# Kernel tuning notes

Measured on AMD Instinct MI355X. Metric: run time of the kernel, lower is better.

The kernel has to match this reference:

```python
import jax, jax.numpy as jnp
import numpy as np

SHAPE = (192, 192, 192)


def _trilinear_sample(img, z, y, x):
    # img: [B,C,D,H,W]; z,y,x: [B,D,H,W] absolute voxel coords (align_corners=True,
    # zero padding outside the volume, matching F.grid_sample defaults in vroc).
    B, C, D, H, W = img.shape
    imgf = img.reshape(B, C, -1)
    z0 = jnp.floor(z); y0 = jnp.floor(y); x0 = jnp.floor(x)
    wz = z - z0; wy = y - y0; wx = x - x0
    z0i = z0.astype(jnp.int32); y0i = y0.astype(jnp.int32); x0i = x0.astype(jnp.int32)
    z1i = z0i + 1; y1i = y0i + 1; x1i = x0i + 1

    def gather(iz, iy, ix):
        valid = ((iz >= 0) & (iz < D) & (iy >= 0) & (iy < H) & (ix >= 0) & (ix < W))
        lin = ((jnp.clip(iz, 0, D - 1) * H + jnp.clip(iy, 0, H - 1)) * W
               + jnp.clip(ix, 0, W - 1)).reshape(B, 1, -1)
        v = jnp.take_along_axis(imgf, jnp.broadcast_to(lin, (B, C, D * H * W)), axis=2)
        return v.reshape(B, C, D, H, W) * valid.reshape(B, 1, D, H, W).astype(img.dtype)

    def w(a, b, c):
        return (a * b * c)[:, None]  # [B,1,D,H,W]

    out = (gather(z0i, y0i, x0i) * w(1 - wz, 1 - wy, 1 - wx)
           + gather(z0i, y0i, x1i) * w(1 - wz, 1 - wy, wx)
           + gather(z0i, y1i, x0i) * w(1 - wz, wy, 1 - wx)
           + gather(z0i, y1i, x1i) * w(1 - wz, wy, wx)
           + gather(z1i, y0i, x0i) * w(wz, 1 - wy, 1 - wx)
           + gather(z1i, y0i, x1i) * w(wz, 1 - wy, wx)
           + gather(z1i, y1i, x0i) * w(wz, wy, 1 - wx)
           + gather(z1i, y1i, x1i) * w(wz, wy, wx))
    return out


def _warp(moving_image, vector_field):
    # SpatialTransformer: identity grid + displacement (voxel units), trilinear sample.
    B, C, D, H, W = moving_image.shape
    dt = moving_image.dtype
    gz, gy, gx = jnp.meshgrid(jnp.arange(D, dtype=dt), jnp.arange(H, dtype=dt),
                              jnp.arange(W, dtype=dt), indexing='ij')
    z = gz[None] + vector_field[:, 0]
    y = gy[None] + vector_field[:, 1]
    x = gx[None] + vector_field[:, 2]
    return _trilinear_sample(moving_image, z, y, x)


def setup_inputs() -> dict:
    key = jax.random.key(0)
    k1, k2, k3, k4 = jax.random.split(key, 4)
    D, H, W = SHAPE
    moving_image = jax.random.normal(k1, (1, 1, D, H, W), dtype=jnp.float32)
    vector_field = jax.random.normal(k2, (1, 3, D, H, W), dtype=jnp.float32) * 3.0
    fixed_image = jax.random.normal(k3, (1, 1, D, H, W), dtype=jnp.float32)
    fixed_image_mask = jax.random.randint(k4, (1, 1, D, H, W), 0, 2).astype(bool)
    return {"moving_image": moving_image, "vector_field": vector_field,
            "fixed_image": fixed_image, "fixed_image_mask": fixed_image_mask}


def reference(moving_image, vector_field, fixed_image, fixed_image_mask):
    warped = _warp(moving_image, vector_field)
    m = fixed_image_mask.astype(warped.dtype)
    sq = (warped - fixed_image) ** 2
    # F.mse_loss(warped[mask], fixed[mask]) == mean of squared diff over masked voxels
    return jnp.sum(sq * m) / jnp.maximum(jnp.sum(m), 1.0)
```

## Files before the change

### kernel.cpp

```cpp
#include <hip/hip_runtime.h>
#include <hip/hip_fp16.h>

#define DD 192
#define HH 192
#define WW 192
#define NVOX (DD * HH * WW)

#define RSX 32
#define RSY 33
#define RSZ 33
#define ROWD 16
#define SLABD (RSY * ROWD)
#define RTOTH (RSX * RSY * RSZ)
#define RTOTD (RTOTH / 2)
#define NCHUNK (RTOTH / 8)
#define CHSLAB (RSY * 4)
#define NT 1024
#define NROUND ((NCHUNK + NT - 1) / NT)
#define NTILE 1728
#define GRID 256

#define AS1 __attribute__((address_space(1)))
#define AS3 __attribute__((address_space(3)))

#define WAITCNT(n) asm volatile("s_waitcnt vmcnt(" #n ")" ::: "memory")

typedef float f32x4 __attribute__((ext_vector_type(4)));
typedef int   i32x4 __attribute__((ext_vector_type(4)));

__global__ __launch_bounds__(256) void conv_fp16(
    const float4* __restrict__ in, int4* __restrict__ out)
{
    const int i = blockIdx.x * 256 + threadIdx.x;
    const float4 a = in[2 * i];
    const float4 b = in[2 * i + 1];
    __half2 h0 = __floats2half2_rn(a.x, a.y);
    __half2 h1 = __floats2half2_rn(a.z, a.w);
    __half2 h2 = __floats2half2_rn(b.x, b.y);
    __half2 h3 = __floats2half2_rn(b.z, b.w);
    int4 o;
    o.x = *(int*)&h0; o.y = *(int*)&h1; o.z = *(int*)&h2; o.w = *(int*)&h3;
    out[i] = o;
}

struct Streams { f32x4 dz, dy, dx, f; i32x4 m; };

__device__ __forceinline__ void tile_coords_oct(
    int n, int OX, int OY, int OZ, int& tx, int& ty, int& tz)
{
    const int ox = n / 36;
    const int r  = n - ox * 36;
    const int oy = r / 6;
    tx = OX + ox;
    ty = OY + oy;
    tz = OZ + (r - oy * 6);
}

__device__ __forceinline__ void stage_tile(
    const ushort* __restrict__ movh, const ushort* __restrict__ zbuf,
    uint* sbufd, int x_lo, int y_lo, int z_lo, int tid)
{
    ushort* sbuf = (ushort*)sbufd;
    #pragma unroll
    for (int i = 0; i < NROUND; ++i) {
        const int q = tid + i * NT;
        if (q < NCHUNK) {
            const int rz = q / CHSLAB;
            const int rem = q - rz * CHSLAB;
            const int ry = rem >> 2;
            const int k  = rem & 3;
            const int gz = z_lo + rz, gy = y_lo + ry, gx = x_lo + 8 * k;
            const bool valid = ((unsigned)gz < DD) & ((unsigned)gy < HH) &
                               ((unsigned)gx < WW);
            const ushort* src = valid ? (movh + ((gz * HH + gy) * WW + gx)) : zbuf;
            const int qb = i * NT + (tid & ~63);
            __builtin_amdgcn_global_load_lds((AS1 void*)src,
                                             (AS3 void*)(sbuf + 8 * qb), 16, 0, 0);
        }
    }
}

__device__ __forceinline__ Streams prefetch_streams(
    const float* __restrict__ vf, const float* __restrict__ fix,
    const int* __restrict__ mask, int base)
{
    Streams s;
    s.dz = __builtin_nontemporal_load((const f32x4*)(vf + base));
    s.dy = __builtin_nontemporal_load((const f32x4*)(vf + NVOX + base));
    s.dx = __builtin_nontemporal_load((const f32x4*)(vf + 2 * NVOX + base));
    s.f  = __builtin_nontemporal_load((const f32x4*)(fix + base));
    s.m  = __builtin_nontemporal_load((const i32x4*)(mask + base));
    return s;
}

__device__ __forceinline__ void sample_accum(
    const uint* sdw, const float* __restrict__ mov,
    int gz, int gy, int gx, float dz, float dy, float dx,
    float f, int m, int x_lo, int y_lo, int z_lo,
    float& sq, float& cnt)
{
    const float z = (float)gz + dz, y = (float)gy + dy, x = (float)gx + dx;
    const float z0f = floorf(z), y0f = floorf(y), x0f = floorf(x);
    const float wz = z - z0f, wy = y - y0f, wx = x - x0f;
    const int z0 = (int)z0f, y0 = (int)y0f, x0 = (int)x0f;
    const int z0l = z0 - z_lo, y0l = y0 - y_lo, x0l = x0 - x_lo;
    const bool inbox = ((unsigned)z0l < RSZ - 1) & ((unsigned)y0l < RSY - 1) &
                       ((unsigned)x0l < RSX - 1);

    float v000, v001, v010, v011, v100, v101, v110, v111;
    if (inbox) {
        const int o = z0l * SLABD + y0l * ROWD + (x0l >> 1);
        const bool odd = (x0l & 1) != 0;
        const uint a00 = sdw[o];
        const uint b00 = sdw[o + 1];
        const uint a01 = sdw[o + ROWD];
        const uint b01 = sdw[o + ROWD + 1];
        const uint a10 = sdw[o + SLABD];
        const uint b10 = sdw[o + SLABD + 1];
        const uint a11 = sdw[o + SLABD + ROWD];
        const uint b11 = sdw[o + SLABD + ROWD + 1];
        auto pr = [&](uint A, uint B, float& l, float& r) {
            const float2 fa = __half22float2(*(const __half2*)&A);
            const float fb = __low2float(*(const __half2*)&B);
            l = odd ? fa.y : fa.x;
            r = odd ? fb   : fa.y;
        };
        pr(a00, b00, v000, v001);
        pr(a01, b01, v010, v011);
        pr(a10, b10, v100, v101);
        pr(a11, b11, v110, v111);
    } else {
        const int z1 = z0 + 1, y1 = y0 + 1, x1 = x0 + 1;
        const bool zi0 = (unsigned)z0 < DD, zi1 = (unsigned)z1 < DD;
        const bool yi0 = (unsigned)y0 < HH, yi1 = (unsigned)y1 < HH;
        const bool xi0 = (unsigned)x0 < WW, xi1 = (unsigned)x1 < WW;
        auto ld = [&](int iz, int iy, int ix, bool ok) -> float {
            return ok ? mov[(iz * HH + iy) * WW + ix] : 0.0f;
        };
        v000 = ld(z0, y0, x0, zi0 & yi0 & xi0);
        v001 = ld(z0, y0, x1, zi0 & yi0 & xi1);
        v010 = ld(z0, y1, x0, zi0 & yi1 & xi0);
        v011 = ld(z0, y1, x1, zi0 & yi1 & xi1);
        v100 = ld(z1, y0, x0, zi1 & yi0 & xi0);
        v101 = ld(z1, y0, x1, zi1 & yi0 & xi1);
        v110 = ld(z1, y1, x0, zi1 & yi1 & xi0);
        v111 = ld(z1, y1, x1, zi1 & yi1 & xi1);
    }

    const float c00 = v000 + (v001 - v000) * wx;
    const float c01 = v010 + (v011 - v010) * wx;
    const float c10 = v100 + (v101 - v100) * wx;
    const float c11 = v110 + (v111 - v110) * wx;
    const float c0 = c00 + (c01 - c00) * wy;
    const float c1 = c10 + (c11 - c10) * wy;
    const float warped = c0 + (c1 - c0) * wz;

    const float mm = (m != 0) ? 1.0f : 0.0f;
    const float diff = warped - f;
    sq += diff * diff * mm;
    cnt += mm;
}

__global__ __launch_bounds__(NT) void warp_mse_persist(
    const ushort* __restrict__ movh,
    const float* __restrict__ mov,
    const float* __restrict__ vf,
    const float* __restrict__ fix,
    const int* __restrict__ mask,
    const ushort* __restrict__ zbuf,
    float* __restrict__ acc,
    float* __restrict__ out)
{
    __shared__ uint sbufd[2][RTOTD];
    __shared__ float s_sq[16], s_cnt[16];

    const int tid = threadIdx.x;
    const int b = blockIdx.x;
    const int xcd = b & 7;
    const int w   = b >> 3;
    const int start = w * 6 + min(w, 24);
    const int cnt_t = 6 + (w < 24 ? 1 : 0);
    const int OX = (xcd & 1) * 6;
    const int OY = ((xcd >> 1) & 1) * 6;
    const int OZ = ((xcd >> 2) & 1) * 6;

    const int lxg = (tid & 3) * 4;
    const int ly  = (tid >> 2) & 15;
    const int lz  = tid >> 6;

    float sq = 0.0f, cntm = 0.0f;

    int tx, ty, tz;
    tile_coords_oct(start, OX, OY, OZ, tx, ty, tz);
    stage_tile(movh, zbuf, sbufd[0], tx * 16 - 8, ty * 16 - 8, tz * 16 - 8, tid);
    Streams Scur = prefetch_streams(vf, fix, mask,
        ((tz * 16 + lz) * HH + ty * 16 + ly) * WW + tx * 16 + lxg);
    Streams Snxt = Scur;
    if (cnt_t > 1) {
        int nx, ny, nz;
        tile_coords_oct(start + 1, OX, OY, OZ, nx, ny, nz);
        stage_tile(movh, zbuf, sbufd[1], nx * 16 - 8, ny * 16 - 8, nz * 16 - 8, tid);
        Snxt = prefetch_streams(vf, fix, mask,
            ((nz * 16 + lz) * HH + ny * 16 + ly) * WW + nx * 16 + lxg);
        WAITCNT(14);
    } else {
        WAITCNT(5);
    }
    __builtin_amdgcn_s_barrier();
    __builtin_amdgcn_sched_barrier(0);

    for (int k = 0; k < cnt_t; ++k) {
        const int cur = k & 1;
        int cx, cy, cz;
        tile_coords_oct(start + k, OX, OY, OZ, cx, cy, cz);
        const int x_lo = cx * 16 - 8, y_lo = cy * 16 - 8, z_lo = cz * 16 - 8;
        const int gz = cz * 16 + lz, gy = cy * 16 + ly, gx0 = cx * 16 + lxg;
        const uint* sdw = sbufd[cur];

        sample_accum(sdw, mov, gz, gy, gx0,     Scur.dz.x, Scur.dy.x, Scur.dx.x,
                     Scur.f.x, Scur.m.x, x_lo, y_lo, z_lo, sq, cntm);
        sample_accum(sdw, mov, gz, gy, gx0 + 1, Scur.dz.y, Scur.dy.y, Scur.dx.y,
                     Scur.f.y, Scur.m.y, x_lo, y_lo, z_lo, sq, cntm);
        sample_accum(sdw, mov, gz, gy, gx0 + 2, Scur.dz.z, Scur.dy.z, Scur.dx.z,
                     Scur.f.z, Scur.m.z, x_lo, y_lo, z_lo, sq, cntm);
        sample_accum(sdw, mov, gz, gy, gx0 + 3, Scur.dz.w, Scur.dy.w, Scur.dx.w,
                     Scur.f.w, Scur.m.w, x_lo, y_lo, z_lo, sq, cntm);

        if (k + 1 < cnt_t) {
            __builtin_amdgcn_sched_barrier(0);
            __builtin_amdgcn_s_barrier();
            Streams Snew = Snxt;
            if (k + 2 < cnt_t) {
                int nx, ny, nz;
                tile_coords_oct(start + k + 2, OX, OY, OZ, nx, ny, nz);
                stage_tile(movh, zbuf, sbufd[cur],
                           nx * 16 - 8, ny * 16 - 8, nz * 16 - 8, tid);
                Snew = prefetch_streams(vf, fix, mask,
                    ((nz * 16 + lz) * HH + ny * 16 + ly) * WW + nx * 16 + lxg);
                WAITCNT(14);
            } else {
                WAITCNT(5);
            }
            __builtin_amdgcn_s_barrier();
            __builtin_amdgcn_sched_barrier(0);
            Scur = Snxt;
            Snxt = Snew;
        }
    }

    #pragma unroll
    for (int off = 32; off > 0; off >>= 1) {
        sq   += __shfl_down(sq, off, 64);
        cntm += __shfl_down(cntm, off, 64);
    }
    const int lane = tid & 63;
    const int wid = tid >> 6;
    if (lane == 0) { s_sq[wid] = sq; s_cnt[wid] = cntm; }
    __syncthreads();
    if (tid == 0) {
        float bsq = 0.0f, bcnt = 0.0f;
        #pragma unroll
        for (int i = 0; i < 16; ++i) { bsq += s_sq[i]; bcnt += s_cnt[i]; }
        atomicAdd(&acc[0], bsq);
        atomicAdd(&acc[1], bcnt);
        __threadfence();
        const unsigned old = atomicAdd((unsigned*)&acc[2], 1u);
        if (old == GRID - 1) {
            __threadfence();
            const float s = atomicAdd(&acc[0], 0.0f);
            const float c = atomicAdd(&acc[1], 0.0f);
            out[0] = s / fmaxf(c, 1.0f);
        }
    }
}

__global__ __launch_bounds__(256) void warp_mse_simple(
    const float* __restrict__ mov, const float* __restrict__ vf,
    const float* __restrict__ fix, const int* __restrict__ mask,
    float* __restrict__ acc)
{
    const int idx = blockIdx.x * 256 + threadIdx.x;
    float sq = 0.0f, cnt = 0.0f;
    if (idx < NVOX) {
        const int w = idx % WW;
        const int t = idx / WW;
        const int h = t % HH;
        const int d = t / HH;
        const float z = (float)d + vf[idx];
        const float y = (float)h + vf[NVOX + idx];
        const float x = (float)w + vf[2 * NVOX + idx];
        const float z0f = floorf(z), y0f = floorf(y), x0f = floorf(x);
        const float wz = z - z0f, wy = y - y0f, wx = x - x0f;
        const int z0 = (int)z0f, y0 = (int)y0f, x0 = (int)x0f;
        const int z1 = z0 + 1, y1 = y0 + 1, x1 = x0 + 1;
        const bool zi0 = (unsigned)z0 < DD, zi1 = (unsigned)z1 < DD;
        const bool yi0 = (unsigned)y0 < HH, yi1 = (unsigned)y1 < HH;
        const bool xi0 = (unsigned)x0 < WW, xi1 = (unsigned)x1 < WW;
        auto ld = [&](int iz, int iy, int ix, bool ok) -> float {
            return ok ? mov[(iz * HH + iy) * WW + ix] : 0.0f;
        };
        const float v000 = ld(z0, y0, x0, zi0 & yi0 & xi0);
        const float v001 = ld(z0, y0, x1, zi0 & yi0 & xi1);
        const float v010 = ld(z0, y1, x0, zi0 & yi1 & xi0);
        const float v011 = ld(z0, y1, x1, zi0 & yi1 & xi1);
        const float v100 = ld(z1, y0, x0, zi1 & yi0 & xi0);
        const float v101 = ld(z1, y0, x1, zi1 & yi0 & xi1);
        const float v110 = ld(z1, y1, x0, zi1 & yi1 & xi0);
        const float v111 = ld(z1, y1, x1, zi1 & yi1 & xi1);
        const float c00 = v000 + (v001 - v000) * wx;
        const float c01 = v010 + (v011 - v010) * wx;
        const float c10 = v100 + (v101 - v100) * wx;
        const float c11 = v110 + (v111 - v110) * wx;
        const float c0 = c00 + (c01 - c00) * wy;
        const float c1 = c10 + (c11 - c10) * wy;
        const float warped = c0 + (c1 - c0) * wz;
        const float m = (mask[idx] != 0) ? 1.0f : 0.0f;
        const float diff = warped - fix[idx];
        sq = diff * diff * m;
        cnt = m;
    }
    #pragma unroll
    for (int off = 32; off > 0; off >>= 1) {
        sq  += __shfl_down(sq, off, 64);
        cnt += __shfl_down(cnt, off, 64);
    }
    __shared__ float s_sq[4], s_cnt[4];
    const int lane = threadIdx.x & 63, wid = threadIdx.x >> 6;
    if (lane == 0) { s_sq[wid] = sq; s_cnt[wid] = cnt; }
    __syncthreads();
    if (threadIdx.x == 0) {
        atomicAdd(&acc[0], s_sq[0] + s_sq[1] + s_sq[2] + s_sq[3]);
        atomicAdd(&acc[1], s_cnt[0] + s_cnt[1] + s_cnt[2] + s_cnt[3]);
    }
}

__global__ void warp_mse_finalize(const float* __restrict__ acc, float* __restrict__ out) {
    out[0] = acc[0] / fmaxf(acc[1], 1.0f);
}

extern "C" void kernel_launch(void* const* d_in, const int* in_sizes, int n_in,
                              void* d_out, int out_size, void* d_ws, size_t ws_size,
                              hipStream_t stream) {
    const float* mov  = (const float*)d_in[0];
    const float* vf   = (const float*)d_in[1];
    const float* fix  = (const float*)d_in[2];
    const int*   mask = (const int*)d_in[3];
    float* acc = (float*)d_ws;
    float* out = (float*)d_out;

    hipMemsetAsync(d_ws, 0, 256, stream);

    const size_t need = 256 + (size_t)NVOX * 2;
    if (ws_size >= need) {
        ushort* movh = (ushort*)((char*)d_ws + 256);
        const ushort* zbuf = (const ushort*)((char*)d_ws + 64);
        conv_fp16<<<NVOX / (256 * 8), 256, 0, stream>>>(
            (const float4*)mov, (int4*)movh);
        warp_mse_persist<<<GRID, NT, 0, stream>>>(movh, mov, vf, fix, mask,
                                                  zbuf, acc, out);
    } else {
        warp_mse_simple<<<(NVOX + 255) / 256, 256, 0, stream>>>(mov, vf, fix, mask, acc);
        warp_mse_finalize<<<1, 1, 0, stream>>>(acc, out);
    }
}
```

Baseline: 233.7 us.

## Reshape tiles to 32x16x8 and use fp16 moving image for fallback gathers

Changes the output tile from 16x16x16 to 32 wide, 16 high and 8 deep. The staged LDS halo region becomes 48x33x25, and the tile indexing, thread mapping and octant offsets are updated to match. The aim is a wider x extent per tile for better coalescing of the streamed inputs and a different halo-to-interior ratio. Out-of-box fallback gathers now read the fp16 copy of the moving image with clamped indices instead of the fp32 copy, which halves the fallback read bytes at some precision cost. The halo volume and per-round chunk counts change, which shifts the LDS footprint and the WAITCNT assumptions that the unchanged vmcnt constants rely on.

New measurement: 217.2 us. -7.1%, faster.

```diff
diff --git a/kernel.cpp b/kernel.cpp
--- a/kernel.cpp
+++ b/kernel.cpp
@@ -6,18 +6,21 @@
 #define WW 192
 #define NVOX (DD * HH * WW)
 
-#define RSX 32
+#define TX 32
+#define TY 16
+#define TZ 8
+#define RSX 48
 #define RSY 33
-#define RSZ 33
-#define ROWD 16
+#define RSZ 25
+#define ROWD 24
 #define SLABD (RSY * ROWD)
 #define RTOTH (RSX * RSY * RSZ)
 #define RTOTD (RTOTH / 2)
 #define NCHUNK (RTOTH / 8)
-#define CHSLAB (RSY * 4)
+#define CHROW 6
+#define CHSLAB (RSY * CHROW)
 #define NT 1024
 #define NROUND ((NCHUNK + NT - 1) / NT)
-#define NTILE 1728
 #define GRID 256
 
 #define AS1 __attribute__((address_space(1)))
@@ -48,12 +51,12 @@
 __device__ __forceinline__ void tile_coords_oct(
     int n, int OX, int OY, int OZ, int& tx, int& ty, int& tz)
 {
-    const int ox = n / 36;
-    const int r  = n - ox * 36;
-    const int oy = r / 6;
+    const int ox = n / 72;
+    const int r  = n - ox * 72;
+    const int oy = r / 12;
     tx = OX + ox;
     ty = OY + oy;
-    tz = OZ + (r - oy * 6);
+    tz = OZ + (r - oy * 12);
 }
 
 __device__ __forceinline__ void stage_tile(
@@ -67,8 +70,8 @@
         if (q < NCHUNK) {
             const int rz = q / CHSLAB;
             const int rem = q - rz * CHSLAB;
-            const int ry = rem >> 2;
-            const int k  = rem & 3;
+            const int ry = rem / CHROW;
+            const int k  = rem - ry * CHROW;
             const int gz = z_lo + rz, gy = y_lo + ry, gx = x_lo + 8 * k;
             const bool valid = ((unsigned)gz < DD) & ((unsigned)gy < HH) &
                                ((unsigned)gx < WW);
@@ -94,7 +97,7 @@
 }
 
 __device__ __forceinline__ void sample_accum(
-    const uint* sdw, const float* __restrict__ mov,
+    const uint* sdw, const ushort* __restrict__ movh,
     int gz, int gy, int gx, float dz, float dy, float dx,
     float f, int m, int x_lo, int y_lo, int z_lo,
     float& sq, float& cnt)
@@ -134,17 +137,21 @@
         const bool zi0 = (unsigned)z0 < DD, zi1 = (unsigned)z1 < DD;
         const bool yi0 = (unsigned)y0 < HH, yi1 = (unsigned)y1 < HH;
         const bool xi0 = (unsigned)x0 < WW, xi1 = (unsigned)x1 < WW;
-        auto ld = [&](int iz, int iy, int ix, bool ok) -> float {
-            return ok ? mov[(iz * HH + iy) * WW + ix] : 0.0f;
-        };
-        v000 = ld(z0, y0, x0, zi0 & yi0 & xi0);
-        v001 = ld(z0, y0, x1, zi0 & yi0 & xi1);
-        v010 = ld(z0, y1, x0, zi0 & yi1 & xi0);
-        v011 = ld(z0, y1, x1, zi0 & yi1 & xi1);
-        v100 = ld(z1, y0, x0, zi1 & yi0 & xi0);
-        v101 = ld(z1, y0, x1, zi1 & yi0 & xi1);
-        v110 = ld(z1, y1, x0, zi1 & yi1 & xi0);
-        v111 = ld(z1, y1, x1, zi1 & yi1 & xi1);
+        const int zc0 = min(max(z0, 0), DD - 1), zc1 = min(max(z1, 0), DD - 1);
+        const int yc0 = min(max(y0, 0), HH - 1), yc1 = min(max(y1, 0), HH - 1);
+        const int xc0 = min(max(x0, 0), WW - 1), xc1 = min(max(x1, 0), WW - 1);
+        const int r00 = (zc0 * HH + yc0) * WW;
+        const int r01 = (zc0 * HH + yc1) * WW;
+        const int r10 = (zc1 * HH + yc0) * WW;
+        const int r11 = (zc1 * HH + yc1) * WW;
+        v000 = (zi0 & yi0 & xi0) ? __half2float(((const __half*)movh)[r00 + xc0]) : 0.0f;
+        v001 = (zi0 & yi0 & xi1) ? __half2float(((const __half*)movh)[r00 + xc1]) : 0.0f;
+        v010 = (zi0 & yi1 & xi0) ? __half2float(((const __half*)movh)[r01 + xc0]) : 0.0f;
+        v011 = (zi0 & yi1 & xi1) ? __half2float(((const __half*)movh)[r01 + xc1]) : 0.0f;
+        v100 = (zi1 & yi0 & xi0) ? __half2float(((const __half*)movh)[r10 + xc0]) : 0.0f;
+        v101 = (zi1 & yi0 & xi1) ? __half2float(((const __half*)movh)[r10 + xc1]) : 0.0f;
+        v110 = (zi1 & yi1 & xi0) ? __half2float(((const __half*)movh)[r11 + xc0]) : 0.0f;
+        v111 = (zi1 & yi1 & xi1) ? __half2float(((const __half*)movh)[r11 + xc1]) : 0.0f;
     }
 
     const float c00 = v000 + (v001 - v000) * wx;
@@ -171,7 +178,7 @@
     float* __restrict__ acc,
     float* __restrict__ out)
 {
-    __shared__ uint sbufd[2][RTOTD];
+    __shared__ uint sbufd[2][RTOTD + 8];
     __shared__ float s_sq[16], s_cnt[16];
 
     const int tid = threadIdx.x;
@@ -180,28 +187,28 @@
     const int w   = b >> 3;
     const int start = w * 6 + min(w, 24);
     const int cnt_t = 6 + (w < 24 ? 1 : 0);
-    const int OX = (xcd & 1) * 6;
+    const int OX = (xcd & 1) * 3;
     const int OY = ((xcd >> 1) & 1) * 6;
-    const int OZ = ((xcd >> 2) & 1) * 6;
-
-    const int lxg = (tid & 3) * 4;
-    const int ly  = (tid >> 2) & 15;
-    const int lz  = tid >> 6;
+    const int OZ = ((xcd >> 2) & 1) * 12;
+
+    const int lxg = (tid & 7) * 4;
+    const int ly  = (tid >> 3) & 15;
+    const int lz  = tid >> 7;
 
     float sq = 0.0f, cntm = 0.0f;
 
     int tx, ty, tz;
     tile_coords_oct(start, OX, OY, OZ, tx, ty, tz);
-    stage_tile(movh, zbuf, sbufd[0], tx * 16 - 8, ty * 16 - 8, tz * 16 - 8, tid);
+    stage_tile(movh, zbuf, sbufd[0], tx * TX - 8, ty * TY - 8, tz * TZ - 8, tid);
     Streams Scur = prefetch_streams(vf, fix, mask,
-        ((tz * 16 + lz) * HH + ty * 16 + ly) * WW + tx * 16 + lxg);
+        ((tz * TZ + lz) * HH + ty * TY + ly) * WW + tx * TX + lxg);
     Streams Snxt = Scur;
     if (cnt_t > 1) {
         int nx, ny, nz;
         tile_coords_oct(start + 1, OX, OY, OZ, nx, ny, nz);
-        stage_tile(movh, zbuf, sbufd[1], nx * 16 - 8, ny * 16 - 8, nz * 16 - 8, tid);
+        stage_tile(movh, zbuf, sbufd[1], nx * TX - 8, ny * TY - 8, nz * TZ - 8, tid);
         Snxt = prefetch_streams(vf, fix, mask,
-            ((nz * 16 + lz) * HH + ny * 16 + ly) * WW + nx * 16 + lxg);
+            ((nz * TZ + lz) * HH + ny * TY + ly) * WW + nx * TX + lxg);
         WAITCNT(14);
     } else {
         WAITCNT(5);
@@ -213,17 +220,17 @@
         const int cur = k & 1;
         int cx, cy, cz;
         tile_coords_oct(start + k, OX, OY, OZ, cx, cy, cz);
-        const int x_lo = cx * 16 - 8, y_lo = cy * 16 - 8, z_lo = cz * 16 - 8;
-        const int gz = cz * 16 + lz, gy = cy * 16 + ly, gx0 = cx * 16 + lxg;
+        const int x_lo = cx * TX - 8, y_lo = cy * TY - 8, z_lo = cz * TZ - 8;
+        const int gz = cz * TZ + lz, gy = cy * TY + ly, gx0 = cx * TX + lxg;
         const uint* sdw = sbufd[cur];
 
-        sample_accum(sdw, mov, gz, gy, gx0,     Scur.dz.x, Scur.dy.x, Scur.dx.x,
+        sample_accum(sdw, movh, gz, gy, gx0,     Scur.dz.x, Scur.dy.x, Scur.dx.x,
                      Scur.f.x, Scur.m.x, x_lo, y_lo, z_lo, sq, cntm);
-        sample_accum(sdw, mov, gz, gy, gx0 + 1, Scur.dz.y, Scur.dy.y, Scur.dx.y,
+        sample_accum(sdw, movh, gz, gy, gx0 + 1, Scur.dz.y, Scur.dy.y, Scur.dx.y,
                      Scur.f.y, Scur.m.y, x_lo, y_lo, z_lo, sq, cntm);
-        sample_accum(sdw, mov, gz, gy, gx0 + 2, Scur.dz.z, Scur.dy.z, Scur.dx.z,
+        sample_accum(sdw, movh, gz, gy, gx0 + 2, Scur.dz.z, Scur.dy.z, Scur.dx.z,
                      Scur.f.z, Scur.m.z, x_lo, y_lo, z_lo, sq, cntm);
-        sample_accum(sdw, mov, gz, gy, gx0 + 3, Scur.dz.w, Scur.dy.w, Scur.dx.w,
+        sample_accum(sdw, movh, gz, gy, gx0 + 3, Scur.dz.w, Scur.dy.w, Scur.dx.w,
                      Scur.f.w, Scur.m.w, x_lo, y_lo, z_lo, sq, cntm);
 
         if (k + 1 < cnt_t) {
@@ -234,9 +241,9 @@
                 int nx, ny, nz;
                 tile_coords_oct(start + k + 2, OX, OY, OZ, nx, ny, nz);
                 stage_tile(movh, zbuf, sbufd[cur],
-                           nx * 16 - 8, ny * 16 - 8, nz * 16 - 8, tid);
+                           nx * TX - 8, ny * TY - 8, nz * TZ - 8, tid);
                 Snew = prefetch_streams(vf, fix, mask,
-                    ((nz * 16 + lz) * HH + ny * 16 + ly) * WW + nx * 16 + lxg);
+                    ((nz * TZ + lz) * HH + ny * TY + ly) * WW + nx * TX + lxg);
                 WAITCNT(14);
             } else {
                 WAITCNT(5);
```
